# Kernel tuning notes

Hardware: AMD Instinct MI355X
Metric: run time of the kernel (lower is better)

## Reference

```python
import jax, jax.numpy as jnp
import numpy as np
from jax import lax

S = 1024  # input_size
G = 10    # grid_size
F = 5     # fiter_size -> 11x11 gaussian kernel
B = 8
C = 3


def _gauss(size, fwhm):
    x = np.arange(size, dtype=np.float64)
    y = x[:, None]
    c = size // 2
    g = np.exp(-4 * np.log(2) * ((x - c) ** 2 + (y - c) ** 2) / fwhm ** 2)
    return (g / g.sum()).astype(np.float32)


def setup_inputs() -> dict:
    key = jax.random.key(0)
    k1, k2, k3 = jax.random.split(key, 3)
    x = jax.random.normal(k1, (B, C, S, S), dtype=jnp.float32)
    offset_x = jax.random.normal(k2, (B, 1, G, G), dtype=jnp.float32)
    offset_y = jax.random.normal(k3, (B, 1, G, G), dtype=jnp.float32)
    weight = jnp.asarray(_gauss(2 * F + 1, F))[None, None]  # [1,1,11,11]
    return {"x": x, "offset_x": offset_x, "offset_y": offset_y,
            "weight": weight, "max_move": 50}


def reference(x, offset_x, offset_y, weight, max_move):
    max_offset = 2.0 * max_move / S

    def smooth(o):  # replication pad + 11x11 gaussian conv + scale + clamp
        p = jnp.pad(o, ((0, 0), (0, 0), (F, F), (F, F)), mode="edge")
        c = lax.conv_general_dilated(p, weight, (1, 1), "VALID",
                                     dimension_numbers=("NCHW", "OIHW", "NCHW"))
        return jnp.clip(c * max_offset, -max_offset, max_offset)

    g = jnp.concatenate([smooth(offset_x), smooth(offset_y)], axis=1)  # [B,2,G,G]

    # bilinear upsample G -> S (align_corners=False, like F.interpolate)
    src = jnp.maximum((jnp.arange(S, dtype=jnp.float32) + 0.5) * (G / S) - 0.5, 0.0)
    i0 = jnp.minimum(jnp.floor(src).astype(jnp.int32), G - 1)
    i1 = jnp.minimum(i0 + 1, G - 1)
    w = src - i0.astype(jnp.float32)
    g = g[:, :, i0, :] * (1 - w)[None, None, :, None] + g[:, :, i1, :] * w[None, None, :, None]
    g = g[:, :, :, i0] * (1 - w) + g[:, :, :, i1] * w  # [B,2,S,S]

    # P basis: channel 0 = x coord, channel 1 = y coord, scaled to [-1,1]
    lin = jnp.arange(S, dtype=jnp.float32) / (S - 1.0)
    P = jnp.stack([jnp.broadcast_to(lin[None, :], (S, S)),
                   jnp.broadcast_to(lin[:, None], (S, S))]) * 2.0 - 1.0
    grid = jnp.clip(g + P, -1.0, 1.0).transpose(0, 2, 3, 1)  # [B,S,S,2] (x,y)

    def gs(img, gr):  # grid_sample bilinear, zeros padding, align_corners=False
        ix = ((gr[..., 0] + 1.0) * S - 1.0) / 2.0
        iy = ((gr[..., 1] + 1.0) * S - 1.0) / 2.0
        x0 = jnp.floor(ix).astype(jnp.int32); x1 = x0 + 1
        y0 = jnp.floor(iy).astype(jnp.int32); y1 = y0 + 1
        wx = ix - x0.astype(ix.dtype)
        wy = iy - y0.astype(iy.dtype)

        def corner(yy, xx, wt):
            v = img[:, jnp.clip(yy, 0, S - 1), jnp.clip(xx, 0, S - 1)]  # [C,S,S]
            m = ((yy >= 0) & (yy < S) & (xx >= 0) & (xx < S)).astype(img.dtype)
            return v * (m * wt)

        return (corner(y0, x0, (1 - wy) * (1 - wx)) + corner(y0, x1, (1 - wy) * wx)
                + corner(y1, x0, wy * (1 - wx)) + corner(y1, x1, wy * wx))

    return jax.vmap(gs)(x, grid)
```

## Files before the change

### kernel.cpp

```cpp
#include <hip/hip_runtime.h>

#define SS 1024
#define GG 10
#define FF 5
#define BB 8
#define CC 3
#define KK (2 * FF + 1)

typedef float f32x2 __attribute__((ext_vector_type(2), aligned(4)));

__global__ __launch_bounds__(256) void rds_smooth_kernel(
    const float* __restrict__ ox, const float* __restrict__ oy,
    const float* __restrict__ w, const void* __restrict__ max_move_p,
    float* __restrict__ gs)
{
    int idx = blockIdx.x * 256 + threadIdx.x;
    if (idx >= BB * 2 * GG * GG) return;
    int j  = idx % GG;
    int i  = (idx / GG) % GG;
    int ch = (idx / (GG * GG)) % 2;
    int b  = idx / (2 * GG * GG);

    const float* o = (ch == 0 ? ox : oy) + b * GG * GG;

    int mi = *(const int*)max_move_p;
    float mv = (mi >= -100000 && mi <= 100000) ? (float)mi : __int_as_float(mi);
    float max_offset = 2.0f * mv / (float)SS;

    float acc = 0.0f;
    for (int u = 0; u < KK; ++u) {
        int yy = min(max(i + u - FF, 0), GG - 1);
        for (int v = 0; v < KK; ++v) {
            int xx = min(max(j + v - FF, 0), GG - 1);
            acc += o[yy * GG + xx] * w[u * KK + v];
        }
    }
    acc *= max_offset;
    acc = fminf(fmaxf(acc, -max_offset), max_offset);
    gs[idx] = acc;
}

__global__ __launch_bounds__(256, 4) void rds_deform_kernel(
    const float* __restrict__ x, const float* __restrict__ gs,
    float* __restrict__ out)
{
    int h     = blockIdx.x;
    int wg    = ((h & 7) << 10) | (h >> 3);
    int xseg  = wg & 3;
    int ytile = (wg >> 2) & 255;
    int b     = wg >> 10;
    int tid   = threadIdx.x;
    int ybase = ytile << 2;
    int xc    = (xseg << 8) + tid;

    __shared__ float rowf[4][2][GG];

    const float GdS = (float)GG / (float)SS;

    if (tid < 80) {
        int p  = tid / 20;
        int r  = tid - p * 20;
        int ch = r / GG;
        int j  = r - ch * GG;
        int y  = ybase + p;
        float sy  = fmaxf(((float)y + 0.5f) * GdS - 0.5f, 0.0f);
        int   i0y = min((int)sy, GG - 1);
        int   i1y = min(i0y + 1, GG - 1);
        float wyu = sy - (float)i0y;
        const float* gb = gs + (b * 2 + ch) * GG * GG;
        rowf[p][ch][j] = gb[i0y * GG + j] + wyu * (gb[i1y * GG + j] - gb[i0y * GG + j]);
    }
    __syncthreads();

    float sx  = fmaxf(((float)xc + 0.5f) * GdS - 0.5f, 0.0f);
    int   i0x = min((int)sx, GG - 1);
    int   i1x = min(i0x + 1, GG - 1);
    float wxu = sx - (float)i0x;
    float pxc = (float)xc * (2.0f / (float)(SS - 1)) - 1.0f;

    int   oa[4], ob[4];
    float wxa[4], wxb[4];
    float wya[4], wyb[4];

    #pragma unroll
    for (int p = 0; p < 4; ++p) {
        float r0a = rowf[p][0][i0x], r0b = rowf[p][0][i1x];
        float r1a = rowf[p][1][i0x], r1b = rowf[p][1][i1x];
        float gxv = r0a + wxu * (r0b - r0a);
        float gyv = r1a + wxu * (r1b - r1a);

        float py  = (float)(ybase + p) * (2.0f / (float)(SS - 1)) - 1.0f;
        float gr0 = fminf(fmaxf(gxv + pxc, -1.0f), 1.0f);
        float gr1 = fminf(fmaxf(gyv + py,  -1.0f), 1.0f);

        float ix = gr0 * 512.0f + 511.5f;
        float iy = gr1 * 512.0f + 511.5f;

        int   x0 = (int)floorf(ix);
        int   y0 = (int)floorf(iy);
        int   y1 = y0 + 1;
        float wx = ix - (float)x0;
        float wy = iy - (float)y0;

        int base = min(max(x0, 0), SS - 2);
        int d    = x0 - base;
        wxa[p] = (d == 0) ? (1.0f - wx) : ((d < 0) ? wx : 0.0f);
        wxb[p] = (d == 0) ? wx          : ((d < 0) ? 0.0f : (1.0f - wx));

        float my0 = ((unsigned)y0 < (unsigned)SS) ? 1.0f : 0.0f;
        float my1 = ((unsigned)y1 < (unsigned)SS) ? 1.0f : 0.0f;
        wya[p] = (1.0f - wy) * my0;
        wyb[p] = wy * my1;

        int cy0 = min(max(y0, 0), SS - 1);
        int cy1 = min(max(y1, 0), SS - 1);
        oa[p] = cy0 * SS + base;
        ob[p] = cy1 * SS + base;
    }

    const float* xb = x + (size_t)b * CC * SS * SS;

    f32x2 la[CC * 4], lb[CC * 4];
    #pragma unroll
    for (int c = 0; c < CC; ++c) {
        const float* img = xb + (size_t)c * SS * SS;
        #pragma unroll
        for (int p = 0; p < 4; ++p) {
            la[c * 4 + p] = *(const f32x2*)(img + oa[p]);
            lb[c * 4 + p] = *(const f32x2*)(img + ob[p]);
        }
    }
    __builtin_amdgcn_sched_barrier(0);

    size_t obase = (((size_t)b * CC) * SS + ybase) * SS + xc;
    #pragma unroll
    for (int c = 0; c < CC; ++c) {
        #pragma unroll
        for (int p = 0; p < 4; ++p) {
            f32x2 fa = la[c * 4 + p];
            f32x2 fb = lb[c * 4 + p];
            float v = wya[p] * (fa.x * wxa[p] + fa.y * wxb[p])
                    + wyb[p] * (fb.x * wxa[p] + fb.y * wxb[p]);
            __builtin_nontemporal_store(
                v, out + obase + (size_t)c * SS * SS + (size_t)(p * SS));
        }
    }
}

extern "C" void kernel_launch(void* const* d_in, const int* in_sizes, int n_in,
                              void* d_out, int out_size, void* d_ws, size_t ws_size,
                              hipStream_t stream) {
    const float* x        = (const float*)d_in[0];
    const float* offset_x = (const float*)d_in[1];
    const float* offset_y = (const float*)d_in[2];
    const float* weight   = (const float*)d_in[3];
    const void*  max_move = d_in[4];
    float* out = (float*)d_out;
    float* gs  = (float*)d_ws;

    int n1 = BB * 2 * GG * GG;
    rds_smooth_kernel<<<(n1 + 255) / 256, 256, 0, stream>>>(
        offset_x, offset_y, weight, max_move, gs);

    int nblocks = BB * (SS / 4) * 4;
    rds_deform_kernel<<<nblocks, 256, 0, stream>>>(x, gs, out);
}
```

Measured before the change: 212.7 us.

## Stage gather loads through LDS via global_load_lds and drop block swizzle

Replaces the register gather of 2-float pairs with direct global-to-LDS loads (global_load_lds, 4 bytes per lane) into a per-wave staging buffer, then reads the values back from LDS. Work is now processed one channel at a time, with an explicit vmcnt wait per channel. The blockIdx swizzle that interleaved batches across workgroups is also removed. The aim is to cut VGPR pressure and use the async LDS load path, but it doubles the number of load instructions and serialises the three channels, which reduces memory-level parallelism.

```diff
diff --git a/kernel.cpp b/kernel.cpp
--- a/kernel.cpp
+++ b/kernel.cpp
@@ -6,8 +6,6 @@
 #define BB 8
 #define CC 3
 #define KK (2 * FF + 1)
-
-typedef float f32x2 __attribute__((ext_vector_type(2), aligned(4)));
 
 __global__ __launch_bounds__(256) void rds_smooth_kernel(
     const float* __restrict__ ox, const float* __restrict__ oy,
@@ -40,20 +38,26 @@
     gs[idx] = acc;
 }
 
+#define GLD4(g, l) __builtin_amdgcn_global_load_lds( \
+    (const __attribute__((address_space(1))) unsigned int*)(const void*)(g), \
+    (__attribute__((address_space(3))) unsigned int*)(void*)(l), 4, 0, 0)
+
 __global__ __launch_bounds__(256, 4) void rds_deform_kernel(
     const float* __restrict__ x, const float* __restrict__ gs,
     float* __restrict__ out)
 {
-    int h     = blockIdx.x;
-    int wg    = ((h & 7) << 10) | (h >> 3);
+    int wg    = blockIdx.x;
     int xseg  = wg & 3;
     int ytile = (wg >> 2) & 255;
     int b     = wg >> 10;
     int tid   = threadIdx.x;
     int ybase = ytile << 2;
     int xc    = (xseg << 8) + tid;
+    int wid   = tid >> 6;
+    int lane  = tid & 63;
 
     __shared__ float rowf[4][2][GG];
+    __shared__ float stage[4 * 16 * 64];
 
     const float GdS = (float)GG / (float)SS;
 
@@ -102,8 +106,8 @@
         float wx = ix - (float)x0;
         float wy = iy - (float)y0;
 
-        int base = min(max(x0, 0), SS - 2);
-        int d    = x0 - base;
+        int bclamp = min(max(x0, 0), SS - 2);
+        int d      = x0 - bclamp;
         wxa[p] = (d == 0) ? (1.0f - wx) : ((d < 0) ? wx : 0.0f);
         wxb[p] = (d == 0) ? wx          : ((d < 0) ? 0.0f : (1.0f - wx));
 
@@ -114,36 +118,41 @@
 
         int cy0 = min(max(y0, 0), SS - 1);
         int cy1 = min(max(y1, 0), SS - 1);
-        oa[p] = cy0 * SS + base;
-        ob[p] = cy1 * SS + base;
+        oa[p] = cy0 * SS + bclamp;
+        ob[p] = cy1 * SS + bclamp;
     }
 
     const float* xb = x + (size_t)b * CC * SS * SS;
+    size_t obase = (((size_t)b * CC) * SS + ybase) * SS + xc;
+    int wbase = wid * (16 * 64);
 
-    f32x2 la[CC * 4], lb[CC * 4];
     #pragma unroll
     for (int c = 0; c < CC; ++c) {
         const float* img = xb + (size_t)c * SS * SS;
+
         #pragma unroll
         for (int p = 0; p < 4; ++p) {
-            la[c * 4 + p] = *(const f32x2*)(img + oa[p]);
-            lb[c * 4 + p] = *(const f32x2*)(img + ob[p]);
+            GLD4(img + oa[p],     &stage[wbase + (2 * p) * 64]);
+            GLD4(img + oa[p] + 1, &stage[wbase + (2 * p + 1) * 64]);
+            GLD4(img + ob[p],     &stage[wbase + (8 + 2 * p) * 64]);
+            GLD4(img + ob[p] + 1, &stage[wbase + (9 + 2 * p) * 64]);
         }
-    }
-    __builtin_amdgcn_sched_barrier(0);
+        asm volatile("s_waitcnt vmcnt(0)" ::: "memory");
+        __builtin_amdgcn_sched_barrier(0);
 
-    size_t obase = (((size_t)b * CC) * SS + ybase) * SS + xc;
-    #pragma unroll
-    for (int c = 0; c < CC; ++c) {
         #pragma unroll
         for (int p = 0; p < 4; ++p) {
-            f32x2 fa = la[c * 4 + p];
-            f32x2 fb = lb[c * 4 + p];
-            float v = wya[p] * (fa.x * wxa[p] + fa.y * wxb[p])
-                    + wyb[p] * (fb.x * wxa[p] + fb.y * wxb[p]);
+            float a0 = stage[wbase + (2 * p) * 64 + lane];
+            float a1 = stage[wbase + (2 * p + 1) * 64 + lane];
+            float b0 = stage[wbase + (8 + 2 * p) * 64 + lane];
+            float b1 = stage[wbase + (9 + 2 * p) * 64 + lane];
+            float v = wya[p] * (a0 * wxa[p] + a1 * wxb[p])
+                    + wyb[p] * (b0 * wxa[p] + b1 * wxb[p]);
             __builtin_nontemporal_store(
                 v, out + obase + (size_t)c * SS * SS + (size_t)(p * SS));
         }
+        asm volatile("s_waitcnt lgkmcnt(0)" ::: "memory");
+        __builtin_amdgcn_sched_barrier(0);
     }
 }
 
```

Result: faster. 206.4 us (-3.0%).
